# Kernel tuning notes

Hardware: AMD Instinct MI355X
Metric: run time of the kernel (lower is better)

Reference implementation:

```python
import jax, jax.numpy as jnp
import numpy as np

C = 256
H = 4  # hard-coded head count in SA_Layer reshapes
EPS = 1e-5


def _bn(x, gamma, beta):
    # training-mode BatchNorm1d over (batch, length) per channel; x: [b,c,n]
    m = jnp.mean(x, axis=(0, 2), keepdims=True)
    v = jnp.var(x, axis=(0, 2), keepdims=True)
    return gamma[None, :, None] * (x - m) * jax.lax.rsqrt(v + EPS) + beta[None, :, None]


def _conv1(w, x, b=None):
    # 1x1 Conv1d == per-point matmul; w: [o,c], x: [b,c,n]
    y = jnp.einsum('oc,bcn->bon', w, x)
    return y if b is None else y + b[None, :, None]


def _sa_layer(x, xyz_emb, qk_w, v_w, v_b, t_w, t_b, bn_g, bn_b):
    b, c, n = x.shape
    h = x + xyz_emb                      # [b,c,n]
    q = _conv1(qk_w, h)                  # [b,c,n]  (q and k share weights)
    # quirky reshape: permute to [b,n,c] then view as [b,H,n,c//H]
    x_q = jnp.transpose(q, (0, 2, 1)).reshape(b, H, n, c // H)
    x_k = q.reshape(b, H, c // H, n)     # standard channel head split
    x_v = _conv1(v_w, h, v_b).reshape(b, H, c // H, n)
    energy = jnp.matmul(x_q, x_k)        # [b,H,n,n]
    att = jax.nn.softmax(energy, axis=-1)
    att = jax.nn.softmax(att, axis=-2)   # dual softmax
    x_r = jnp.matmul(x_v, att).reshape(b, c, n)
    x_r = jax.nn.relu(_bn(_conv1(t_w, x - x_r, t_b), bn_g, bn_b))
    return x + x_r


def setup_inputs() -> dict:
    key = jax.random.key(0)
    ks = jax.random.split(key, 16)
    B, N = 4, 2048
    s = 1.0 / np.sqrt(C)
    inp = {
        'x': jax.random.normal(ks[0], (B, C, N), jnp.float32),
        'xyz': jax.random.normal(ks[1], (B, N, 3), jnp.float32),
        'conv1_w': jax.random.normal(ks[2], (C, C), jnp.float32) * s,
        'pos_w': jax.random.normal(ks[3], (C, 3), jnp.float32) * 0.5,
        'pos_b': jax.random.normal(ks[4], (C,), jnp.float32) * 0.02,
        'bn1_g': jnp.ones((C,), jnp.float32),
        'bn1_b': jnp.zeros((C,), jnp.float32),
        'qk_w': jax.random.normal(ks[5], (4, C, C), jnp.float32) * s,
        'v_w': jax.random.normal(ks[6], (4, C, C), jnp.float32) * s,
        'v_b': jax.random.normal(ks[7], (4, C), jnp.float32) * 0.02,
        't_w': jax.random.normal(ks[8], (4, C, C), jnp.float32) * s,
        't_b': jax.random.normal(ks[9], (4, C), jnp.float32) * 0.02,
        'bn_g': jnp.ones((4, C), jnp.float32),
        'bn_b': jnp.zeros((4, C), jnp.float32),
    }
    return inp


def reference(x, xyz, conv1_w, pos_w, pos_b, bn1_g, bn1_b,
              qk_w, v_w, v_b, t_w, t_b, bn_g, bn_b):
    # xyz: [B,N,3] -> permute -> pos_xyz (1x1 conv)
    xyz_emb = jnp.einsum('oi,bni->bon', pos_w, xyz) + pos_b[None, :, None]  # [b,C,n]
    h = jax.nn.relu(_bn(_conv1(conv1_w, x), bn1_g, bn1_b))
    outs = []
    for i in range(4):
        h = _sa_layer(h, xyz_emb, qk_w[i], v_w[i], v_b[i],
                      t_w[i], t_b[i], bn_g[i], bn_b[i])
        outs.append(h)
    return jnp.concatenate(outs, axis=1)  # [b, 4*C, n]
```

## Files before the change

### kernel.cpp

```cpp
#include <hip/hip_runtime.h>
#include <math.h>

#define Bsz 4
#define Cch 256
#define Npt 2048
#define Hh  4
#define NL  4
#define BN_CNT (Bsz * Npt)
#define EPSV 1e-5f
#define NROW (16 * Npt)
#define L2E 1.44269504f

typedef _Float16 f16x8 __attribute__((ext_vector_type(8)));
typedef _Float16 f16x4 __attribute__((ext_vector_type(4)));
typedef float    f32x4 __attribute__((ext_vector_type(4)));

__device__ __forceinline__ float fexp2(float x) { return __builtin_amdgcn_exp2f(x); }

__device__ __forceinline__ void gld16(const _Float16* g, _Float16* l) {
    __builtin_amdgcn_global_load_lds(
        (const __attribute__((address_space(1))) unsigned int*)g,
        (__attribute__((address_space(3))) unsigned int*)l, 16, 0, 0);
}

__global__ void k_xyz_emb(const float* __restrict__ xyz, const float* __restrict__ pw,
                          const float* __restrict__ pb, float* __restrict__ emb) {
    int idx = blockIdx.x * 256 + threadIdx.x;
    int n = idx & (Npt - 1);
    int c = (idx >> 11) & (Cch - 1);
    int b = idx >> 19;
    const float* xz = xyz + (b * Npt + n) * 3;
    emb[idx] = pw[c * 3 + 0] * xz[0] + pw[c * 3 + 1] * xz[1] + pw[c * 3 + 2] * xz[2] + pb[c];
}

__global__ void k_castw(const float* __restrict__ c1w, const float* __restrict__ qkw,
                        const float* __restrict__ vw, const float* __restrict__ tw,
                        _Float16* __restrict__ o, float* __restrict__ bnacc) {
    int i = blockIdx.x * 256 + threadIdx.x;
    if (i < 5 * 512) bnacc[i] = 0.f;
    const float* src; int off;
    if (i < 65536)            { src = c1w; off = i; }
    else if (i < 327680)      { src = qkw; off = i - 65536; }
    else if (i < 589824)      { src = vw;  off = i - 327680; }
    else                      { src = tw;  off = i - 589824; }
    o[i] = (_Float16)src[off];
}

__global__ __launch_bounds__(256) void k_fuse_t(const float* __restrict__ in,
        _Float16* __restrict__ XT) {
    __shared__ _Float16 Tt[64][72];
    const int b = blockIdx.z, c0 = blockIdx.y * 64, n0 = blockIdx.x * 64;
    const int t = threadIdx.x;
    const int cl = t >> 2, ns = (t & 3) * 16;
    const float* ip = in + ((size_t)(b * Cch + c0 + cl) * Npt) + n0 + ns;
    #pragma unroll
    for (int g = 0; g < 4; ++g) {
        float4 v = *(const float4*)(ip + g * 4);
        Tt[ns + g * 4 + 0][cl] = (_Float16)v.x;
        Tt[ns + g * 4 + 1][cl] = (_Float16)v.y;
        Tt[ns + g * 4 + 2][cl] = (_Float16)v.z;
        Tt[ns + g * 4 + 3][cl] = (_Float16)v.w;
    }
    __syncthreads();
    int nl = t >> 2, cs = (t & 3) * 16;
    _Float16* op = XT + ((size_t)(b * Npt + n0 + nl) * Cch) + c0 + cs;
    #pragma unroll
    for (int g = 0; g < 4; ++g)
        *(f16x4*)(op + g * 4) = *(f16x4*)&Tt[nl][cs + g * 4];
}

__global__ __launch_bounds__(256) void k_gemm_mfma(const _Float16* __restrict__ Wb,
        const _Float16* __restrict__ XT, const float* __restrict__ bias,
        float* __restrict__ Yf, float* __restrict__ bnacc) {
    __shared__ float EpF[64][68];
    const int b = blockIdx.z, o0 = blockIdx.y * 64, n0 = blockIdx.x * 64;
    const int tid = threadIdx.x, w = tid >> 6, quad = (tid >> 4) & 3, tx = tid & 15;
    const _Float16* Arow = Wb + (o0 + w * 16 + tx) * Cch + quad * 8;
    const _Float16* Brow = XT + ((size_t)(b * Npt + n0 + tx) * Cch) + quad * 8;
    f32x4 acc[4];
    #pragma unroll
    for (int s = 0; s < 4; ++s) acc[s] = (f32x4){0.f, 0.f, 0.f, 0.f};
    for (int k0 = 0; k0 < Cch; k0 += 32) {
        f16x8 a = *(const f16x8*)(Arow + k0);
        #pragma unroll
        for (int s = 0; s < 4; ++s) {
            f16x8 bb = *(const f16x8*)(Brow + s * 16 * Cch + k0);
            acc[s] = __builtin_amdgcn_mfma_f32_16x16x32_f16(a, bb, acc[s], 0, 0, 0);
        }
    }
    float bv[4];
    {
        int ob = o0 + w * 16 + quad * 4;
        if (bias) { bv[0] = bias[ob]; bv[1] = bias[ob + 1]; bv[2] = bias[ob + 2]; bv[3] = bias[ob + 3]; }
        else bv[0] = bv[1] = bv[2] = bv[3] = 0.f;
    }
    #pragma unroll
    for (int s = 0; s < 4; ++s) {
        int ol = w * 16 + quad * 4, nl = s * 16 + tx;
        EpF[ol + 0][nl] = acc[s][0] + bv[0];
        EpF[ol + 1][nl] = acc[s][1] + bv[1];
        EpF[ol + 2][nl] = acc[s][2] + bv[2];
        EpF[ol + 3][nl] = acc[s][3] + bv[3];
    }
    __syncthreads();
    int row = tid >> 2, seg = (tid & 3) * 16;
    float* yp = Yf + ((size_t)(b * Cch + o0 + row) * Npt) + n0 + seg;
    float s1 = 0.f, s2 = 0.f;
    #pragma unroll
    for (int g = 0; g < 4; ++g) {
        float4 v = *(float4*)&EpF[row][seg + g * 4];
        *(float4*)(yp + g * 4) = v;
        s1 += v.x + v.y + v.z + v.w;
        s2 += v.x * v.x + v.y * v.y + v.z * v.z + v.w * v.w;
    }
    s1 += __shfl_xor(s1, 1); s2 += __shfl_xor(s2, 1);
    s1 += __shfl_xor(s1, 2); s2 += __shfl_xor(s2, 2);
    if ((tid & 3) == 0) {
        atomicAdd(&bnacc[o0 + row], s1);
        atomicAdd(&bnacc[256 + o0 + row], s2);
    }
}

__global__ __launch_bounds__(256) void k_gemm_qkv(const _Float16* __restrict__ Wqk,
        const _Float16* __restrict__ Wv, const _Float16* __restrict__ XT,
        const float* __restrict__ vbias, _Float16* __restrict__ Vb,
        _Float16* __restrict__ Qg, _Float16* __restrict__ Kt) {
    __shared__ _Float16 EpB[64][72];
    const int b = blockIdx.z, y = blockIdx.y, n0 = blockIdx.x * 64;
    const int isV = (y >= 4);
    const int o0 = (isV ? (y - 4) : y) * 64;
    const _Float16* Wb = isV ? Wv : Wqk;
    const int tid = threadIdx.x, w = tid >> 6, quad = (tid >> 4) & 3, tx = tid & 15;
    const _Float16* Arow = Wb + (o0 + w * 16 + tx) * Cch + quad * 8;
    const _Float16* Brow = XT + ((size_t)(b * Npt + n0 + tx) * Cch) + quad * 8;
    f32x4 acc[4];
    #pragma unroll
    for (int s = 0; s < 4; ++s) acc[s] = (f32x4){0.f, 0.f, 0.f, 0.f};
    for (int k0 = 0; k0 < Cch; k0 += 32) {
        f16x8 a = *(const f16x8*)(Arow + k0);
        #pragma unroll
        for (int s = 0; s < 4; ++s) {
            f16x8 bb = *(const f16x8*)(Brow + s * 16 * Cch + k0);
            acc[s] = __builtin_amdgcn_mfma_f32_16x16x32_f16(a, bb, acc[s], 0, 0, 0);
        }
    }
    if (!isV) {
        const int cch = (w << 1) + (quad >> 1);
        const int hof = (quad & 1) * 4;
        #pragma unroll
        for (int s = 0; s < 4; ++s) {
            int ng = n0 + s * 16 + tx;
            f16x4 pk;
            pk[0] = (_Float16)acc[s][0]; pk[1] = (_Float16)acc[s][1];
            pk[2] = (_Float16)acc[s][2]; pk[3] = (_Float16)acc[s][3];
            int rK = ng & 63, jt = ng >> 6;
            size_t ka = ((size_t)((b * Hh + (o0 >> 6)) * 32 + jt) << 12)
                      + rK * 64 + ((cch ^ (rK & 7)) * 8) + hof;
            *(f16x4*)&Kt[ka] = pk;
            int iQ = ((ng & 511) << 2) + (o0 >> 6);
            int rQ = iQ & 63, it = iQ >> 6;
            size_t qa = ((size_t)((b * Hh + (ng >> 9)) * 32 + it) << 12)
                      + rQ * 64 + ((cch ^ (rQ & 7)) * 8) + hof;
            *(f16x4*)&Qg[qa] = pk;
        }
        return;
    }
    float bv[4];
    {
        int ob = o0 + w * 16 + quad * 4;
        bv[0] = vbias[ob]; bv[1] = vbias[ob + 1]; bv[2] = vbias[ob + 2]; bv[3] = vbias[ob + 3];
    }
    #pragma unroll
    for (int s = 0; s < 4; ++s) {
        int ol = w * 16 + quad * 4, nl = s * 16 + tx;
        EpB[ol + 0][nl] = (_Float16)(acc[s][0] + bv[0]);
        EpB[ol + 1][nl] = (_Float16)(acc[s][1] + bv[1]);
        EpB[ol + 2][nl] = (_Float16)(acc[s][2] + bv[2]);
        EpB[ol + 3][nl] = (_Float16)(acc[s][3] + bv[3]);
    }
    __syncthreads();
    int row = tid >> 2, seg = (tid & 3) * 16;
    const int m = tid & 3;
    const int pbase = (m >> 1) * 32 + (m & 1) * 4;
    _Float16* yp = Vb + ((size_t)(b * Cch + o0 + row) * Npt) + n0 + pbase;
    #pragma unroll
    for (int g = 0; g < 4; ++g)
        *(f16x4*)(yp + g * 8) = *(f16x4*)&EpB[row][seg + g * 4];
}

__global__ __launch_bounds__(256) void k_attn_A(const _Float16* __restrict__ Qg,
        const _Float16* __restrict__ Kt, float* __restrict__ mP, float* __restrict__ lP) {
    __shared__ _Float16 Ksh[2][4096];
    const int flat = blockIdx.x;
    const int bh = (flat & 7) * 2 + ((flat >> 3) & 1);
    const int rest = flat >> 4;
    const int i0 = (rest & 15) * 128;
    const int jc = rest >> 4;
    const int tid = threadIdx.x, w = tid >> 6, q = (tid >> 4) & 3, tx = tid & 15;
    const int lane = tid & 63;
    const int sx = tx & 7;
    f16x8 qa[2][2];
    #pragma unroll
    for (int g = 0; g < 2; ++g) {
        const _Float16* Qtile = Qg + ((size_t)(bh * 32 + ((i0 + g * 64) >> 6)) << 12);
        int r = w * 16 + tx;
        qa[g][0] = *(const f16x8*)(Qtile + r * 64 + (q ^ sx) * 8);
        qa[g][1] = *(const f16x8*)(Qtile + r * 64 + ((q + 4) ^ sx) * 8);
    }
    const _Float16* Kbase = Kt + ((size_t)(bh * 32) << 12);
    const int jt0 = jc * 8;
    {
        const _Float16* g = Kbase + ((size_t)jt0 << 12) + (w * 2) * 512 + lane * 8;
        gld16(g,       &Ksh[0][(w * 2 + 0) * 512]);
        gld16(g + 512, &Ksh[0][(w * 2 + 1) * 512]);
    }
    __syncthreads();
    float m2[2][4], l[2][4];
    #pragma unroll
    for (int g = 0; g < 2; ++g)
        #pragma unroll
        for (int r = 0; r < 4; ++r) { m2[g][r] = -1e30f; l[g][r] = 0.f; }
    for (int t = 0; t < 8; ++t) {
        if (t < 7) {
            const _Float16* g = Kbase + ((size_t)(jt0 + t + 1) << 12) + (w * 2) * 512 + lane * 8;
            gld16(g,       &Ksh[(t + 1) & 1][(w * 2 + 0) * 512]);
            gld16(g + 512, &Ksh[(t + 1) & 1][(w * 2 + 1) * 512]);
        }
        const _Float16* kbuf = Ksh[t & 1];
        f32x4 e[2][4];
        #pragma unroll
        for (int s = 0; s < 4; ++s) {
            int r = s * 16 + tx;
            f16x8 kb0 = *(const f16x8*)(kbuf + r * 64 + (q ^ sx) * 8);
            f16x8 kb1 = *(const f16x8*)(kbuf + r * 64 + ((q + 4) ^ sx) * 8);
            #pragma unroll
            for (int g = 0; g < 2; ++g) {
                f32x4 z = (f32x4){0.f, 0.f, 0.f, 0.f};
                z = __builtin_amdgcn_mfma_f32_16x16x32_f16(qa[g][0], kb0, z, 0, 0, 0);
                e[g][s] = __builtin_amdgcn_mfma_f32_16x16x32_f16(qa[g][1], kb1, z, 0, 0, 0);
            }
        }
        #pragma unroll
        for (int g = 0; g < 2; ++g)
            #pragma unroll
            for (int r = 0; r < 4; ++r) {
                float e0 = e[g][0][r] * L2E, e1 = e[g][1][r] * L2E;
                float e2 = e[g][2][r] * L2E, e3 = e[g][3][r] * L2E;
                float lm = fmaxf(fmaxf(e0, e1), fmaxf(e2, e3));
                float nm = fmaxf(m2[g][r], lm);
                l[g][r] = l[g][r] * fexp2(m2[g][r] - nm)
                        + fexp2(e0 - nm) + fexp2(e1 - nm) + fexp2(e2 - nm) + fexp2(e3 - nm);
                m2[g][r] = nm;
            }
        __syncthreads();
    }
    #pragma unroll
    for (int g = 0; g < 2; ++g)
        #pragma unroll
        for (int r = 0; r < 4; ++r) {
            float mm = m2[g][r], ll = l[g][r];
            #pragma unroll
            for (int off = 1; off < 16; off <<= 1) {
                float om = __shfl_xor(mm, off), ol = __shfl_xor(ll, off);
                float nm = fmaxf(mm, om);
                ll = ll * fexp2(mm - nm) + ol * fexp2(om - nm);
                mm = nm;
            }
            if (tx == 0) {
                int idx = bh * Npt + i0 + g * 64 + w * 16 + q * 4 + r;
                mP[jc * NROW + idx] = mm;
                lP[jc * NROW + idx] = ll;
            }
        }
}

__global__ __launch_bounds__(512, 4) void k_attn_B(const _Float16* __restrict__ Qg,
        const _Float16* __restrict__ Kt, const _Float16* __restrict__ Vb,
        const float* __restrict__ mP, const float* __restrict__ lP,
        const float* __restrict__ h, _Float16* __restrict__ XT) {
    __shared__ float mlm[Npt];
    __shared__ float mll[Npt];
    __shared__ float Ssh[8][32];
    __shared__ _Float16 TS[8][2048];
    const int flat = blockIdx.x;
    const int bh = (flat & 7) * 2 + ((flat >> 3) & 1);
    const int j0 = (flat >> 4) * 64;
    const int b = bh >> 2, hd = bh & 3;
    const int tid = threadIdx.x, w = tid >> 6, q = (tid >> 4) & 3, tx = tid & 15;
    const int sx = tx & 7;
    const int jh = w >> 2;
    const int wq = w & 3;
    {
        const int ii = tid * 4;
        const int idx = bh * Npt + ii;
        float4 m0 = *(const float4*)&mP[idx];
        float4 m1 = *(const float4*)&mP[NROW + idx];
        float4 m2 = *(const float4*)&mP[2 * NROW + idx];
        float4 m3 = *(const float4*)&mP[3 * NROW + idx];
        float4 l0 = *(const float4*)&lP[idx];
        float4 l1 = *(const float4*)&lP[NROW + idx];
        float4 l2 = *(const float4*)&lP[2 * NROW + idx];
        float4 l3 = *(const float4*)&lP[3 * NROW + idx];
        #pragma unroll
        for (int k = 0; k < 4; ++k) {
            float a0 = ((const float*)&m0)[k], a1 = ((const float*)&m1)[k];
            float a2 = ((const float*)&m2)[k], a3 = ((const float*)&m3)[k];
            float mm = fmaxf(fmaxf(a0, a1), fmaxf(a2, a3));
            float ll = ((const float*)&l0)[k] * fexp2(a0 - mm)
                     + ((const float*)&l1)[k] * fexp2(a1 - mm)
                     + ((const float*)&l2)[k] * fexp2(a2 - mm)
                     + ((const float*)&l3)[k] * fexp2(a3 - mm);
            mlm[ii + k] = mm;
            mll[ii + k] = L2E / ll;
        }
    }
    f16x8 kb[2][2];
    {
        const _Float16* Ktile = Kt + ((size_t)(bh * 32 + (j0 >> 6)) << 12);
        #pragma unroll
        for (int nt = 0; nt < 2; ++nt) {
            int r = jh * 32 + nt * 16 + tx;
            kb[nt][0] = *(const f16x8*)(Ktile + r * 64 + (q ^ sx) * 8);
            kb[nt][1] = *(const f16x8*)(Ktile + r * 64 + ((q + 4) ^ sx) * 8);
        }
    }
    __syncthreads();
    f32x4 Tacc[4][2];
    #pragma unroll
    for (int mt = 0; mt < 4; ++mt)
        #pragma unroll
        for (int nt = 0; nt < 2; ++nt) Tacc[mt][nt] = (f32x4){0.f, 0.f, 0.f, 0.f};
    float scS[2] = {0.f, 0.f};
    const _Float16* vbase = Vb + (size_t)(b * Cch + hd * 64) * Npt;
    for (int it = 0; it < 8; ++it) {
        const int i0 = wq * 512 + it * 64;
        const _Float16* Qtile = Qg + ((size_t)(bh * 32 + (i0 >> 6)) << 12);
        #pragma unroll
        for (int pp = 0; pp < 2; ++pp) {
            f16x4 pk[2][2];
            #pragma unroll
            for (int mt2 = 0; mt2 < 2; ++mt2) {
                const int mt = pp * 2 + mt2;
                const int r = mt * 16 + tx;
                f16x8 qa0 = *(const f16x8*)(Qtile + r * 64 + (q ^ sx) * 8);
                f16x8 qa1 = *(const f16x8*)(Qtile + r * 64 + ((q + 4) ^ sx) * 8);
                float4 m2v = *(const float4*)&mlm[i0 + mt * 16 + q * 4];
                float4 liv = *(const float4*)&mll[i0 + mt * 16 + q * 4];
                #pragma unroll
                for (int nt = 0; nt < 2; ++nt) {
                    f32x4 z = (f32x4){0.f, 0.f, 0.f, 0.f};
                    z = __builtin_amdgcn_mfma_f32_16x16x32_f16(qa0, kb[nt][0], z, 0, 0, 0);
                    z = __builtin_amdgcn_mfma_f32_16x16x32_f16(qa1, kb[nt][1], z, 0, 0, 0);
                    float a0 = fexp2(fexp2(__builtin_fmaf(z[0], L2E, -m2v.x)) * liv.x);
                    float a1 = fexp2(fexp2(__builtin_fmaf(z[1], L2E, -m2v.y)) * liv.y);
                    float a2 = fexp2(fexp2(__builtin_fmaf(z[2], L2E, -m2v.z)) * liv.z);
                    float a3 = fexp2(fexp2(__builtin_fmaf(z[3], L2E, -m2v.w)) * liv.w);
                    scS[nt] += a0 + a1 + a2 + a3;
                    f16x4 pkk;
                    pkk[0] = (_Float16)a0; pkk[1] = (_Float16)a1;
                    pkk[2] = (_Float16)a2; pkk[3] = (_Float16)a3;
                    pk[mt2][nt] = pkk;
                }
            }
            #pragma unroll
            for (int mtd = 0; mtd < 4; ++mtd) {
                f16x8 va = *(const f16x8*)(vbase + (size_t)(mtd * 16 + tx) * Npt + i0 + pp * 32 + q * 8);
                #pragma unroll
                for (int nt = 0; nt < 2; ++nt) {
                    f16x8 pb = __builtin_shufflevector(pk[0][nt], pk[1][nt], 0, 1, 2, 3, 4, 5, 6, 7);
                    Tacc[mtd][nt] = __builtin_amdgcn_mfma_f32_16x16x32_f16(va, pb, Tacc[mtd][nt], 0, 0, 0);
                }
            }
        }
    }
    #pragma unroll
    for (int nt = 0; nt < 2; ++nt) {
        float s = scS[nt];
        s += __shfl_xor(s, 16);
        s += __shfl_xor(s, 32);
        if (q == 0) Ssh[w][nt * 16 + tx] = s;
    }
    #pragma unroll
    for (int mtd = 0; mtd < 4; ++mtd)
        #pragma unroll
        for (int nt = 0; nt < 2; ++nt) {
            f16x4 pkk;
            pkk[0] = (_Float16)Tacc[mtd][nt][0];
            pkk[1] = (_Float16)Tacc[mtd][nt][1];
            pkk[2] = (_Float16)Tacc[mtd][nt][2];
            pkk[3] = (_Float16)Tacc[mtd][nt][3];
            *(f16x4*)&TS[w][(nt * 16 + tx) * 64 + ((2 * mtd + (q >> 1)) ^ sx) * 8 + (q & 1) * 4] = pkk;
        }
    __syncthreads();
    {
        const int jl = tid >> 3, d8 = tid & 7;
        const int wb = (jl >> 5) * 4;
        const int jj = jl & 31;
        const int tsbase = jj * 64 + ((d8 ^ (jj & 7)) * 8);
        f16x8 t0 = *(const f16x8*)&TS[wb + 0][tsbase];
        f16x8 t1 = *(const f16x8*)&TS[wb + 1][tsbase];
        f16x8 t2 = *(const f16x8*)&TS[wb + 2][tsbase];
        f16x8 t3 = *(const f16x8*)&TS[wb + 3][tsbase];
        const float s4 = Ssh[wb + 0][jj] + Ssh[wb + 1][jj] + Ssh[wb + 2][jj] + Ssh[wb + 3][jj];
        const float rs = 1.f / s4;
        const int jg = j0 + jl;
        const float* hp = h + ((size_t)(b * Cch + hd * 64 + d8 * 8) * Npt) + jg;
        f16x8 u;
        #pragma unroll
        for (int e = 0; e < 8; ++e) {
            float tv = (float)t0[e] + (float)t1[e] + (float)t2[e] + (float)t3[e];
            u[e] = (_Float16)(hp[(size_t)e * Npt] - tv * rs);
        }
        *(f16x8*)(XT + ((size_t)(b * Npt + jg) * Cch) + hd * 64 + d8 * 8) = u;
    }
}

__global__ __launch_bounds__(256) void k_bn_fuse(const float* __restrict__ t,
        const float* __restrict__ bnacc,
        const float* __restrict__ g, const float* __restrict__ bt,
        const float* __restrict__ emb, const float* __restrict__ resid,
        float* __restrict__ hout, float* __restrict__ out, _Float16* __restrict__ XT,
        int layer) {
    __shared__ _Float16 Tt[64][72];
    const int b = blockIdx.z, c0 = blockIdx.y * 64, n0 = blockIdx.x * 64;
    const int tt = threadIdx.x;
    const int cl = tt >> 2, ns = (tt & 3) * 16;
    const int c = c0 + cl;
    const float mn = bnacc[c] * (1.f / BN_CNT);
    const float var = bnacc[256 + c] * (1.f / BN_CNT) - mn * mn;
    const float is = rsqrtf(var + EPSV);
    const float gg = g[c], bb = bt[c];
    const size_t rowoff = ((size_t)(b * Cch + c) * Npt) + n0 + ns;
    const float* tp = t + rowoff;
    const float* ep = emb + rowoff;
    const float* rp = resid ? resid + rowoff : nullptr;
    float* hp = hout + rowoff;
    float* op = out ? out + (size_t)b * (NL * Cch * Npt) + (size_t)(layer * Cch + c) * Npt + n0 + ns
                    : nullptr;
    #pragma unroll
    for (int gi = 0; gi < 4; ++gi) {
        float4 v = *(const float4*)(tp + gi * 4);
        float4 y;
        y.x = fmaxf(gg * (v.x - mn) * is + bb, 0.f);
        y.y = fmaxf(gg * (v.y - mn) * is + bb, 0.f);
        y.z = fmaxf(gg * (v.z - mn) * is + bb, 0.f);
        y.w = fmaxf(gg * (v.w - mn) * is + bb, 0.f);
        if (rp) {
            float4 r = *(const float4*)(rp + gi * 4);
            y.x += r.x; y.y += r.y; y.z += r.z; y.w += r.w;
        }
        *(float4*)(hp + gi * 4) = y;
        if (op) *(float4*)(op + gi * 4) = y;
        float4 e = *(const float4*)(ep + gi * 4);
        Tt[ns + gi * 4 + 0][cl] = (_Float16)(y.x + e.x);
        Tt[ns + gi * 4 + 1][cl] = (_Float16)(y.y + e.y);
        Tt[ns + gi * 4 + 2][cl] = (_Float16)(y.z + e.z);
        Tt[ns + gi * 4 + 3][cl] = (_Float16)(y.w + e.w);
    }
    __syncthreads();
    int nl = tt >> 2, cs = (tt & 3) * 16;
    _Float16* xp = XT + ((size_t)(b * Npt + n0 + nl) * Cch) + c0 + cs;
    #pragma unroll
    for (int gi = 0; gi < 4; ++gi)
        *(f16x4*)(xp + gi * 4) = *(f16x4*)&Tt[nl][cs + gi * 4];
}

extern "C" void kernel_launch(void* const* d_in, const int* in_sizes, int n_in,
                              void* d_out, int out_size, void* d_ws, size_t ws_size,
                              hipStream_t stream) {
    (void)in_sizes; (void)n_in; (void)out_size; (void)ws_size;
    const float* x    = (const float*)d_in[0];
    const float* xyz  = (const float*)d_in[1];
    const float* c1w  = (const float*)d_in[2];
    const float* posw = (const float*)d_in[3];
    const float* posb = (const float*)d_in[4];
    const float* bn1g = (const float*)d_in[5];
    const float* bn1b = (const float*)d_in[6];
    const float* qkw  = (const float*)d_in[7];
    const float* vw   = (const float*)d_in[8];
    const float* vb   = (const float*)d_in[9];
    const float* tw   = (const float*)d_in[10];
    const float* tb   = (const float*)d_in[11];
    const float* bng  = (const float*)d_in[12];
    const float* bnb  = (const float*)d_in[13];
    float* out = (float*)d_out;

    const size_t NE = (size_t)Bsz * Cch * Npt;
    char* W = (char*)d_ws;
    float* emb   = (float*)W;                 W += NE * 4;
    float* h     = (float*)W;                 W += NE * 4;
    float* vbuf  = (float*)W;                 W += NE * 4;
    _Float16* XT = (_Float16*)W;              W += NE * 2;
    _Float16* Qg = (_Float16*)W;              W += NE * 2;
    _Float16* Kt = (_Float16*)W;              W += NE * 2;
    _Float16* Vb = (_Float16*)W;              W += NE * 2;
    _Float16* wbf = (_Float16*)W;             W += 851968 * 2;
    float* mP    = (float*)W;                 W += 4 * NROW * 4;
    float* lP    = (float*)W;                 W += 4 * NROW * 4;
    float* bnacc = (float*)W;                 W += 5 * 512 * 4;

    dim3 blk(256);
    dim3 g4(Npt / 64, Cch / 64, Bsz);
    dim3 gQKV(Npt / 64, 8, Bsz);
    int ew = (int)(NE / 256);

    k_castw<<<3328, blk, 0, stream>>>(c1w, qkw, vw, tw, wbf, bnacc);
    k_xyz_emb<<<ew, blk, 0, stream>>>(xyz, posw, posb, emb);

    k_fuse_t<<<g4, blk, 0, stream>>>(x, XT);
    k_gemm_mfma<<<g4, blk, 0, stream>>>(wbf, XT, nullptr, vbuf, bnacc);
    k_bn_fuse<<<g4, blk, 0, stream>>>(vbuf, bnacc, bn1g, bn1b, emb, nullptr,
                                      h, nullptr, XT, 0);

    for (int L = 0; L < NL; ++L) {
        const _Float16* qkL = wbf + 65536 + (size_t)L * 65536;
        const _Float16* vL  = wbf + 327680 + (size_t)L * 65536;
        const _Float16* tL  = wbf + 589824 + (size_t)L * 65536;
        float* accL = bnacc + (1 + L) * 512;
        k_gemm_qkv<<<gQKV, blk, 0, stream>>>(qkL, vL, XT, vb + L * Cch, Vb, Qg, Kt);
        k_attn_A<<<1024, blk, 0, stream>>>(Qg, Kt, mP, lP);
        k_attn_B<<<512, dim3(512), 0, stream>>>(Qg, Kt, Vb, mP, lP, h, XT);
        k_gemm_mfma<<<g4, blk, 0, stream>>>(tL, XT, tb + L * Cch, vbuf, accL);
        k_bn_fuse<<<g4, blk, 0, stream>>>(vbuf, accL, bng + L * Cch, bnb + L * Cch,
                                          emb, h, h, out, XT, L);
    }
}
```

Before: 615.3 us.

## Rework attn_B to four waves each covering all 64 output columns

Reorganizes the second attention kernel from 8 waves (two column halves × four row quarters) to 4 waves that each process all 64 columns over a quarter of the rows. Each Q tile and its softmax statistics are reused across twice as many columns, reducing redundant loads. The cost is doubled accumulator registers and a smaller block with lower declared occupancy, which may reduce latency hiding.

```diff
diff --git a/kernel.cpp b/kernel.cpp
--- a/kernel.cpp
+++ b/kernel.cpp
@@ -274,70 +274,72 @@
         }
 }
 
-__global__ __launch_bounds__(512, 4) void k_attn_B(const _Float16* __restrict__ Qg,
+__global__ __launch_bounds__(256, 2) void k_attn_B(const _Float16* __restrict__ Qg,
         const _Float16* __restrict__ Kt, const _Float16* __restrict__ Vb,
         const float* __restrict__ mP, const float* __restrict__ lP,
         const float* __restrict__ h, _Float16* __restrict__ XT) {
     __shared__ float mlm[Npt];
     __shared__ float mll[Npt];
-    __shared__ float Ssh[8][32];
-    __shared__ _Float16 TS[8][2048];
+    __shared__ float Ssh[4][64];
+    __shared__ _Float16 TS[4][4096];
     const int flat = blockIdx.x;
     const int bh = (flat & 7) * 2 + ((flat >> 3) & 1);
     const int j0 = (flat >> 4) * 64;
     const int b = bh >> 2, hd = bh & 3;
     const int tid = threadIdx.x, w = tid >> 6, q = (tid >> 4) & 3, tx = tid & 15;
     const int sx = tx & 7;
-    const int jh = w >> 2;
-    const int wq = w & 3;
     {
-        const int ii = tid * 4;
-        const int idx = bh * Npt + ii;
-        float4 m0 = *(const float4*)&mP[idx];
-        float4 m1 = *(const float4*)&mP[NROW + idx];
-        float4 m2 = *(const float4*)&mP[2 * NROW + idx];
-        float4 m3 = *(const float4*)&mP[3 * NROW + idx];
-        float4 l0 = *(const float4*)&lP[idx];
-        float4 l1 = *(const float4*)&lP[NROW + idx];
-        float4 l2 = *(const float4*)&lP[2 * NROW + idx];
-        float4 l3 = *(const float4*)&lP[3 * NROW + idx];
-        #pragma unroll
-        for (int k = 0; k < 4; ++k) {
-            float a0 = ((const float*)&m0)[k], a1 = ((const float*)&m1)[k];
-            float a2 = ((const float*)&m2)[k], a3 = ((const float*)&m3)[k];
-            float mm = fmaxf(fmaxf(a0, a1), fmaxf(a2, a3));
-            float ll = ((const float*)&l0)[k] * fexp2(a0 - mm)
-                     + ((const float*)&l1)[k] * fexp2(a1 - mm)
-                     + ((const float*)&l2)[k] * fexp2(a2 - mm)
-                     + ((const float*)&l3)[k] * fexp2(a3 - mm);
-            mlm[ii + k] = mm;
-            mll[ii + k] = L2E / ll;
-        }
-    }
-    f16x8 kb[2][2];
+        const int ib = tid * 8;
+        #pragma unroll
+        for (int e = 0; e < 2; ++e) {
+            int ii = ib + e * 4;
+            int idx = bh * Npt + ii;
+            float4 m0 = *(const float4*)&mP[idx];
+            float4 m1 = *(const float4*)&mP[NROW + idx];
+            float4 m2 = *(const float4*)&mP[2 * NROW + idx];
+            float4 m3 = *(const float4*)&mP[3 * NROW + idx];
+            float4 l0 = *(const float4*)&lP[idx];
+            float4 l1 = *(const float4*)&lP[NROW + idx];
+            float4 l2 = *(const float4*)&lP[2 * NROW + idx];
+            float4 l3 = *(const float4*)&lP[3 * NROW + idx];
+            #pragma unroll
+            for (int k = 0; k < 4; ++k) {
+                float a0 = ((const float*)&m0)[k], a1 = ((const float*)&m1)[k];
+                float a2 = ((const float*)&m2)[k], a3 = ((const float*)&m3)[k];
+                float mm = fmaxf(fmaxf(a0, a1), fmaxf(a2, a3));
+                float ll = ((const float*)&l0)[k] * fexp2(a0 - mm)
+                         + ((const float*)&l1)[k] * fexp2(a1 - mm)
+                         + ((const float*)&l2)[k] * fexp2(a2 - mm)
+                         + ((const float*)&l3)[k] * fexp2(a3 - mm);
+                mlm[ii + k] = mm;
+                mll[ii + k] = L2E / ll;
+            }
+        }
+    }
+    f16x8 kb[4][2];
     {
         const _Float16* Ktile = Kt + ((size_t)(bh * 32 + (j0 >> 6)) << 12);
         #pragma unroll
-        for (int nt = 0; nt < 2; ++nt) {
-            int r = jh * 32 + nt * 16 + tx;
+        for (int nt = 0; nt < 4; ++nt) {
+            int r = nt * 16 + tx;
             kb[nt][0] = *(const f16x8*)(Ktile + r * 64 + (q ^ sx) * 8);
             kb[nt][1] = *(const f16x8*)(Ktile + r * 64 + ((q + 4) ^ sx) * 8);
         }
     }
     __syncthreads();
-    f32x4 Tacc[4][2];
+    f32x4 Tacc[4][4];
     #pragma unroll
     for (int mt = 0; mt < 4; ++mt)
         #pragma unroll
-        for (int nt = 0; nt < 2; ++nt) Tacc[mt][nt] = (f32x4){0.f, 0.f, 0.f, 0.f};
-    float scS[2] = {0.f, 0.f};
+        for (int nt = 0; nt < 4; ++nt) Tacc[mt][nt] = (f32x4){0.f, 0.f, 0.f, 0.f};
+    float scS[4] = {0.f, 0.f, 0.f, 0.f};
     const _Float16* vbase = Vb + (size_t)(b * Cch + hd * 64) * Npt;
     for (int it = 0; it < 8; ++it) {
-        const int i0 = wq * 512 + it * 64;
+        const int i0 = w * 512 + it * 64;
         const _Float16* Qtile = Qg + ((size_t)(bh * 32 + (i0 >> 6)) << 12);
         #pragma unroll
         for (int pp = 0; pp < 2; ++pp) {
-            f16x4 pk[2][2];
+            f16x4 pk[2][4];
             #pragma unroll
             for (int mt2 = 0; mt2 < 2; ++mt2) {
                 const int mt = pp * 2 + mt2;
@@ -347,7 +349,7 @@
                 float4 m2v = *(const float4*)&mlm[i0 + mt * 16 + q * 4];
                 float4 liv = *(const float4*)&mll[i0 + mt * 16 + q * 4];
                 #pragma unroll
-                for (int nt = 0; nt < 2; ++nt) {
+                for (int nt = 0; nt < 4; ++nt) {
                     f32x4 z = (f32x4){0.f, 0.f, 0.f, 0.f};
                     z = __builtin_amdgcn_mfma_f32_16x16x32_f16(qa0, kb[nt][0], z, 0, 0, 0);
                     z = __builtin_amdgcn_mfma_f32_16x16x32_f16(qa1, kb[nt][1], z, 0, 0, 0);
@@ -366,7 +368,7 @@
             for (int mtd = 0; mtd < 4; ++mtd) {
                 f16x8 va = *(const f16x8*)(vbase + (size_t)(mtd * 16 + tx) * Npt + i0 + pp * 32 + q * 8);
                 #pragma unroll
-                for (int nt = 0; nt < 2; ++nt) {
+                for (int nt = 0; nt < 4; ++nt) {
                     f16x8 pb = __builtin_shufflevector(pk[0][nt], pk[1][nt], 0, 1, 2, 3, 4, 5, 6, 7);
                     Tacc[mtd][nt] = __builtin_amdgcn_mfma_f32_16x16x32_f16(va, pb, Tacc[mtd][nt], 0, 0, 0);
                 }
@@ -374,7 +376,7 @@
         }
     }
     #pragma unroll
-    for (int nt = 0; nt < 2; ++nt) {
+    for (int nt = 0; nt < 4; ++nt) {
         float s = scS[nt];
         s += __shfl_xor(s, 16);
         s += __shfl_xor(s, 32);
@@ -383,7 +385,7 @@
     #pragma unroll
     for (int mtd = 0; mtd < 4; ++mtd)
         #pragma unroll
-        for (int nt = 0; nt < 2; ++nt) {
+        for (int nt = 0; nt < 4; ++nt) {
             f16x4 pkk;
             pkk[0] = (_Float16)Tacc[mtd][nt][0];
             pkk[1] = (_Float16)Tacc[mtd][nt][1];
@@ -393,25 +395,27 @@
         }
     __syncthreads();
     {
-        const int jl = tid >> 3, d8 = tid & 7;
-        const int wb = (jl >> 5) * 4;
-        const int jj = jl & 31;
-        const int tsbase = jj * 64 + ((d8 ^ (jj & 7)) * 8);
-        f16x8 t0 = *(const f16x8*)&TS[wb + 0][tsbase];
-        f16x8 t1 = *(const f16x8*)&TS[wb + 1][tsbase];
-        f16x8 t2 = *(const f16x8*)&TS[wb + 2][tsbase];
-        f16x8 t3 = *(const f16x8*)&TS[wb + 3][tsbase];
-        const float s4 = Ssh[wb + 0][jj] + Ssh[wb + 1][jj] + Ssh[wb + 2][jj] + Ssh[wb + 3][jj];
+        const int jl = tid >> 2, d4 = tid & 3;
+        const float s4 = Ssh[0][jl] + Ssh[1][jl] + Ssh[2][jl] + Ssh[3][jl];
         const float rs = 1.f / s4;
         const int jg = j0 + jl;
-        const float* hp = h + ((size_t)(b * Cch + hd * 64 + d8 * 8) * Npt) + jg;
-        f16x8 u;
-        #pragma unroll
-        for (int e = 0; e < 8; ++e) {
-            float tv = (float)t0[e] + (float)t1[e] + (float)t2[e] + (float)t3[e];
-            u[e] = (_Float16)(hp[(size_t)e * Npt] - tv * rs);
-        }
-        *(f16x8*)(XT + ((size_t)(b * Npt + jg) * Cch) + hd * 64 + d8 * 8) = u;
+        #pragma unroll
+        for (int g = 0; g < 2; ++g) {
+            const int s8 = d4 * 2 + g;
+            const int base = jl * 64 + ((s8 ^ (jl & 7)) * 8);
+            f16x8 t0 = *(const f16x8*)&TS[0][base];
+            f16x8 t1 = *(const f16x8*)&TS[1][base];
+            f16x8 t2 = *(const f16x8*)&TS[2][base];
+            f16x8 t3 = *(const f16x8*)&TS[3][base];
+            const float* hp = h + ((size_t)(b * Cch + hd * 64 + s8 * 8) * Npt) + jg;
+            f16x8 u;
+            #pragma unroll
+            for (int e = 0; e < 8; ++e) {
+                float tv = (float)t0[e] + (float)t1[e] + (float)t2[e] + (float)t3[e];
+                u[e] = (_Float16)(hp[(size_t)e * Npt] - tv * rs);
+            }
+            *(f16x8*)(XT + ((size_t)(b * Npt + jg) * Cch) + hd * 64 + s8 * 8) = u;
+        }
     }
 }
 
@@ -519,7 +523,7 @@
         float* accL = bnacc + (1 + L) * 512;
         k_gemm_qkv<<<gQKV, blk, 0, stream>>>(qkL, vL, XT, vb + L * Cch, Vb, Qg, Kt);
         k_attn_A<<<1024, blk, 0, stream>>>(Qg, Kt, mP, lP);
-        k_attn_B<<<512, dim3(512), 0, stream>>>(Qg, Kt, Vb, mP, lP, h, XT);
+        k_attn_B<<<512, blk, 0, stream>>>(Qg, Kt, Vb, mP, lP, h, XT);
         k_gemm_mfma<<<g4, blk, 0, stream>>>(tL, XT, tb + L * Cch, vbuf, accL);
         k_bn_fuse<<<g4, blk, 0, stream>>>(vbuf, accL, bng + L * Cch, bnb + L * Cch,
                                           emb, h, h, out, XT, L);
```

Result: faster. 558.6 us (-9.2%).
